# Optimization experiments

Measured on AMD Instinct MI355X. Metric: run time of the kernel, lower is better.

Reference implementation:

```python
import jax, jax.numpy as jnp
import numpy as np

K = 3  # kernel_size


def conv2d_same(x, w, b):
    # x: NHWC, w: HWIO
    y = jax.lax.conv_general_dilated(
        x, w, window_strides=(1, 1), padding='SAME',
        dimension_numbers=('NHWC', 'HWIO', 'NHWC'))
    return y + b


def setup_inputs() -> dict:
    key = jax.random.key(0)
    k0, k1, k2 = jax.random.split(key, 3)
    B, H, Wd, C, F = 8, 128, 128, 64, 128
    x = jax.random.normal(k0, (B, H, Wd, C), jnp.float32)
    # offset conv: small random weights (zeros in original init -> degenerate),
    # scaled down so offsets stay in a realistic few-pixel range
    W_off = jax.random.normal(k1, (K, K, C, 2 * K * K), jnp.float32) * 0.01
    b_off = jnp.zeros((2 * K * K,), jnp.float32)
    fan_in = K * K * K * K * C
    W = jax.random.normal(k2, (K, K, K * K * C, F), jnp.float32) / np.float32(np.sqrt(fan_in))
    b = jnp.zeros((F,), jnp.float32)
    return {"x": x, "W_off": W_off, "b_off": b_off, "W": W, "b": b}


def reference(x, W_off, b_off, W, b):
    B, H, Wd, C = x.shape
    KK = K * K
    # predicted per-pixel, per-tap (dx, dy) offsets
    offsets = conv2d_same(x, W_off, b_off).reshape(B, H, Wd, KK, 2)

    # base pixel grid, stacked as (x, y) like the original
    gy, gx = jnp.meshgrid(jnp.arange(H, dtype=jnp.float32),
                          jnp.arange(Wd, dtype=jnp.float32), indexing='ij')
    grid = jnp.stack([gx, gy], axis=-1)[None, :, :, None, :]  # (1,H,W,1,2)

    # kernel tap grid, 'xy' meshgrid like tf.meshgrid default
    off = (K - 1) / 2.0
    lin = jnp.linspace(-off, off, K).astype(jnp.float32)
    kx, ky = jnp.meshgrid(lin, lin)
    kgrid = jnp.stack([kx, ky], axis=-1).reshape(1, 1, 1, KK, 2)

    loc = grid + kgrid + offsets  # (B,H,W,KK,2)
    lx = jnp.clip(loc[..., 0], 0.0, Wd - 1.0)
    ly = jnp.clip(loc[..., 1], 0.0, H - 1.0)

    x0 = jnp.clip(jnp.floor(lx), 0.0, Wd - 1.0)
    x1 = jnp.clip(jnp.floor(lx) + 1.0, 0.0, Wd - 1.0)
    y0 = jnp.clip(jnp.floor(ly), 0.0, H - 1.0)
    y1 = jnp.clip(jnp.floor(ly) + 1.0, 0.0, H - 1.0)

    # weights computed from the CLIPPED corner coords, as in the original
    wa = (x1 - lx) * (y1 - ly)
    wb = (x1 - lx) * (ly - y0)
    wc = (lx - x0) * (y1 - ly)
    wd = (lx - x0) * (ly - y0)

    x0i, x1i = x0.astype(jnp.int32), x1.astype(jnp.int32)
    y0i, y1i = y0.astype(jnp.int32), y1.astype(jnp.int32)

    xf = x.reshape(B, H * Wd, C)

    def gather(yi, xi):
        idx = (yi * Wd + xi).reshape(B, -1)           # (B, H*W*KK)
        g = jax.vmap(lambda f, i: f[i])(xf, idx)      # (B, P, C)
        return g.reshape(B, H, Wd, KK, C)

    Ia = gather(y0i, x0i)
    Ib = gather(y1i, x0i)
    Ic = gather(y0i, x1i)
    Id = gather(y1i, x1i)

    sampled = (wa[..., None] * Ia + wb[..., None] * Ib
               + wc[..., None] * Ic + wd[..., None] * Id)
    sampled = sampled.reshape(B, H, Wd, KK * C)
    return conv2d_same(sampled, W, b)
```

## Files before the change

### kernel.cpp

```cpp
#include <hip/hip_runtime.h>
#include <hip/hip_bf16.h>

#define B_   8
#define H_   128
#define W_   128
#define C_   64
#define F_   128
#define KDIM 5184
#define BHW_ 131072

#define TH   8
#define TW   16
#define HY   10
#define HX   18
#define NPX  180

#define STILE 0
#define BTILE 11520
#define PARMW 36096
#define PARMO 37536
#define LDSSZ 38976

typedef __bf16 bf16x8 __attribute__((ext_vector_type(8)));
typedef float  f32x4  __attribute__((ext_vector_type(4)));

__device__ __forceinline__ unsigned short f2bf(float f) {
  unsigned int u = __float_as_uint(f);
  unsigned int r = (u + 0x7fffu + ((u >> 16) & 1u)) >> 16;
  return (unsigned short)r;
}

__global__ __launch_bounds__(256) void woff_prep_kernel(
    const float* __restrict__ Woff, unsigned short* __restrict__ WbHi,
    unsigned short* __restrict__ WbLo) {
  int u = blockIdx.x * 256 + threadIdx.x;
  if (u >= 18432) return;
  int j  = u & 7;
  int kq = (u >> 3) & 3;
  int n  = (u >> 5) & 15;
  int nt = (u >> 9) & 1;
  int tc = u >> 10;
  int tap = tc >> 1, kch = tc & 1;
  int o = nt * 16 + n;
  int c = kch * 32 + kq * 8 + j;
  float val = 0.f;
  if (o < 18) val = Woff[(tap * 64 + c) * 18 + o];
  unsigned short h = f2bf(val);
  float hf = __uint_as_float((unsigned)h << 16);
  WbHi[u] = h;
  WbLo[u] = f2bf(val - hf);
}

__global__ __launch_bounds__(256, 3) void offs_mfma_kernel(
    const float* __restrict__ x, const unsigned short* __restrict__ WbHi,
    const unsigned short* __restrict__ WbLo, const float* __restrict__ boff,
    float* __restrict__ offsP) {
  __shared__ __align__(16) short lds[26112];
  const int tid = threadIdx.x, lane = tid & 63, w = tid >> 6;
  const int bid = blockIdx.x;
  const int b  = bid >> 7;
  const int t  = bid & 127;
  const int r4 = t >> 2, cq = t & 3;
  const int gy0 = r4 * 4, gx0 = cq * 32;
  const float* xb = x + (size_t)b * (H_ * W_ * C_);

#pragma unroll
  for (int it = 0; it < 7; ++it) {
    int u = it * 256 + tid;
    if (u < 1632) {
      int p = u >> 3, j = u & 7;
      int rowi = p / 34, coli = p - rowi * 34;
      int gy = gy0 - 1 + rowi, gx = gx0 - 1 + coli;
      union { unsigned short s[8]; uint4 v; } hi, lo;
      if ((unsigned)gy < (unsigned)H_ && (unsigned)gx < (unsigned)W_) {
        const float* src = xb + (((gy << 7) + gx) << 6) + j * 8;
        float4 v0 = ((const float4*)src)[0], v1 = ((const float4*)src)[1];
        float f[8] = {v0.x, v0.y, v0.z, v0.w, v1.x, v1.y, v1.z, v1.w};
#pragma unroll
        for (int e = 0; e < 8; ++e) {
          unsigned short h16 = f2bf(f[e]);
          hi.s[e] = h16;
          lo.s[e] = f2bf(f[e] - __uint_as_float((unsigned)h16 << 16));
        }
      } else {
        hi.v = make_uint4(0, 0, 0, 0);
        lo.v = hi.v;
      }
      int a = p * 64 + ((j ^ (coli & 7)) * 8);
      *(uint4*)&lds[a] = hi.v;
      *(uint4*)&lds[13056 + a] = lo.v;
    }
  }
  __syncthreads();

  const int l15 = lane & 15, kq = lane >> 4;
  const int bbase = (l15 * 4 + kq) * 8;
  f32x4 acc[2][2] = {};

#pragma unroll
  for (int ky = 0; ky < 3; ++ky) {
#pragma unroll
    for (int kx = 0; kx < 3; ++kx) {
      const int tap = ky * 3 + kx;
#pragma unroll
      for (int kch = 0; kch < 2; ++kch) {
        const int tc = tap * 2 + kch;
        bf16x8 bh0 = *(const bf16x8*)&WbHi[tc * 1024 + bbase];
        bf16x8 bh1 = *(const bf16x8*)&WbHi[tc * 1024 + 512 + bbase];
        bf16x8 bl0 = *(const bf16x8*)&WbLo[tc * 1024 + bbase];
        bf16x8 bl1 = *(const bf16x8*)&WbLo[tc * 1024 + 512 + bbase];
#pragma unroll
        for (int mt = 0; mt < 2; ++mt) {
          int coli = mt * 16 + l15 + kx;
          int px = (w + ky) * 34 + coli;
          int a = px * 64 + (((kch * 4 + kq) ^ (coli & 7)) * 8);
          bf16x8 ah = *(const bf16x8*)&lds[a];
          bf16x8 al = *(const bf16x8*)&lds[13056 + a];
          acc[mt][0] = __builtin_amdgcn_mfma_f32_16x16x32_bf16(ah, bh0, acc[mt][0], 0, 0, 0);
          acc[mt][0] = __builtin_amdgcn_mfma_f32_16x16x32_bf16(al, bh0, acc[mt][0], 0, 0, 0);
          acc[mt][0] = __builtin_amdgcn_mfma_f32_16x16x32_bf16(ah, bl0, acc[mt][0], 0, 0, 0);
          acc[mt][1] = __builtin_amdgcn_mfma_f32_16x16x32_bf16(ah, bh1, acc[mt][1], 0, 0, 0);
          acc[mt][1] = __builtin_amdgcn_mfma_f32_16x16x32_bf16(al, bh1, acc[mt][1], 0, 0, 0);
          acc[mt][1] = __builtin_amdgcn_mfma_f32_16x16x32_bf16(ah, bl1, acc[mt][1], 0, 0, 0);
        }
      }
    }
  }

  __syncthreads();
  float* accbuf = (float*)lds;
  float bv0 = boff[l15];
  float bv1 = boff[min(16 + l15, 17)];
#pragma unroll
  for (int mt = 0; mt < 2; ++mt)
#pragma unroll
    for (int r = 0; r < 4; ++r) {
      int px = mt * 16 + kq * 4 + r;
      accbuf[(w * 32 + px) * 19 + l15] = acc[mt][0][r] + bv0;
      if (l15 < 2)
        accbuf[(w * 32 + px) * 19 + 16 + l15] = acc[mt][1][r] + bv1;
    }
  __syncthreads();
  const int lane32 = tid & 31, tpi = tid >> 5;
#pragma unroll
  for (int v = 0; v < 9; ++v) {
    int u = v * 8 + tpi;
    int o = u >> 2, w2 = u & 3;
    float val = accbuf[(w2 * 32 + lane32) * 19 + o];
    offsP[(size_t)o * BHW_ + (size_t)b * 16384 + (gy0 + w2) * 128 + gx0 + lane32] = val;
  }
}

__global__ __launch_bounds__(256) void wt_prep_kernel(
    const float* __restrict__ Wf, unsigned short* __restrict__ Wt) {
  __shared__ float Wl[64][65];
  const int tid = threadIdx.x;
  const int kk0 = (blockIdx.x % 81) * 64;
  const int f0  = (blockIdx.x / 81) * 64;
  for (int i = tid; i < 4096; i += 256) {
    int kk = i >> 6, f = i & 63;
    Wl[kk][f] = Wf[(size_t)(kk0 + kk) * F_ + f0 + f];
  }
  __syncthreads();
  for (int i = tid; i < 4096; i += 256) {
    int f = i >> 6, kk = i & 63;
    Wt[(size_t)(f0 + f) * KDIM + kk0 + kk] = f2bf(Wl[kk][f]);
  }
}

__global__ __launch_bounds__(256, 2) void fused_kernel(
    const float* __restrict__ x, const float* __restrict__ offsP,
    const unsigned short* __restrict__ Wt, const float* __restrict__ bias,
    float* __restrict__ out) {
  __shared__ __align__(16) short lds[LDSSZ];
  const int tid  = threadIdx.x;
  const int lane = tid & 63;
  const int wv   = tid >> 6;
  const int gr   = (blockIdx.x & 7) * 128 + (blockIdx.x >> 3);
  const int b    = gr >> 7;
  const int tile = gr & 127;
  const int ty   = tile >> 3, tx = tile & 7;
  const int gy0  = ty * TH, gx0 = tx * TW;
  const float* xb = x + (size_t)b * (H_ * W_ * C_);

  const int l15  = lane & 15, quad = lane >> 4;
  const int sub  = lane & 7,  rig  = lane >> 3;
  const int wm   = (wv >> 1) * 64, wn = (wv & 1) * 64;

  f32x4 acc[4][4] = {};

  int p0[4];
#pragma unroll
  for (int i = 0; i < 4; ++i) p0[i] = ((wv >> 1) * 4 + i) * HX + l15;
  int bo[2][4];
#pragma unroll
  for (int ks = 0; ks < 2; ++ks)
#pragma unroll
    for (int j = 0; j < 4; ++j)
      bo[ks][j] = BTILE + (wn + 16 * j + l15) * 64 + (((ks * 4 + quad) ^ (l15 & 7)) * 8);

  const int s_py = tid / HX, s_px = tid - s_py * HX;

  for (int t = 0; t < 9; ++t) {
    __syncthreads();
    if (tid < NPX) {
      int gy = gy0 + s_py - 1, gx = gx0 + s_px - 1;
      float wa = 0.f, wb = 0.f, wc = 0.f, wd = 0.f;
      int oA = 0, oB = 0, oC = 0, oD = 0;
      if ((unsigned)gy < (unsigned)H_ && (unsigned)gx < (unsigned)W_) {
        int pix = (b * H_ + gy) * W_ + gx;
        float offx = offsP[(size_t)(2 * t) * BHW_ + pix];
        float offy = offsP[(size_t)(2 * t + 1) * BHW_ + pix];
        float lx = (float)gx + (float)(t % 3 - 1) + offx;
        float ly = (float)gy + (float)(t / 3 - 1) + offy;
        lx = fminf(fmaxf(lx, 0.f), 127.f);
        ly = fminf(fmaxf(ly, 0.f), 127.f);
        float fx = floorf(lx), fy = floorf(ly);
        float x0c = fminf(fmaxf(fx, 0.f), 127.f);
        float x1c = fminf(fmaxf(fx + 1.f, 0.f), 127.f);
        float y0c = fminf(fmaxf(fy, 0.f), 127.f);
        float y1c = fminf(fmaxf(fy + 1.f, 0.f), 127.f);
        wa = (x1c - lx) * (y1c - ly);
        wb = (x1c - lx) * (ly - y0c);
        wc = (lx - x0c) * (y1c - ly);
        wd = (lx - x0c) * (ly - y0c);
        int ix0 = (int)x0c, ix1 = (int)x1c, iy0 = (int)y0c, iy1 = (int)y1c;
        oA = (iy0 * W_ + ix0) * C_;
        oB = (iy1 * W_ + ix0) * C_;
        oC = (iy0 * W_ + ix1) * C_;
        oD = (iy1 * W_ + ix1) * C_;
      }
      ((float4*)&lds[PARMW])[tid] = make_float4(wa, wb, wc, wd);
      ((int4*)&lds[PARMO])[tid]  = make_int4(oA | (s_px << 20), oB, oC, oD);
    }
    __syncthreads();
#pragma unroll
    for (int it = 0; it < 6; ++it) {
      int u = it * 256 + tid;
      if (u < NPX * 8) {
        int p = u >> 3, j = u & 7;
        float4 wv4 = ((const float4*)&lds[PARMW])[p];
        int4   ov4 = ((const int4*)&lds[PARMO])[p];
        int pxl = ov4.x >> 20;
        const float* pa = xb + (ov4.x & 0xFFFFF) + j * 8;
        const float* pb = xb + ov4.y + j * 8;
        const float* pc = xb + ov4.z + j * 8;
        const float* pd = xb + ov4.w + j * 8;
        float4 A0 = ((const float4*)pa)[0], A1 = ((const float4*)pa)[1];
        float4 B0 = ((const float4*)pb)[0], B1 = ((const float4*)pb)[1];
        float4 C0 = ((const float4*)pc)[0], C1 = ((const float4*)pc)[1];
        float4 D0 = ((const float4*)pd)[0], D1 = ((const float4*)pd)[1];
        union { unsigned short s[8]; uint4 v; } uu;
        uu.s[0] = f2bf(wv4.x * A0.x + wv4.y * B0.x + wv4.z * C0.x + wv4.w * D0.x);
        uu.s[1] = f2bf(wv4.x * A0.y + wv4.y * B0.y + wv4.z * C0.y + wv4.w * D0.y);
        uu.s[2] = f2bf(wv4.x * A0.z + wv4.y * B0.z + wv4.z * C0.z + wv4.w * D0.z);
        uu.s[3] = f2bf(wv4.x * A0.w + wv4.y * B0.w + wv4.z * C0.w + wv4.w * D0.w);
        uu.s[4] = f2bf(wv4.x * A1.x + wv4.y * B1.x + wv4.z * C1.x + wv4.w * D1.x);
        uu.s[5] = f2bf(wv4.x * A1.y + wv4.y * B1.y + wv4.z * C1.y + wv4.w * D1.y);
        uu.s[6] = f2bf(wv4.x * A1.z + wv4.y * B1.z + wv4.z * C1.z + wv4.w * D1.z);
        uu.s[7] = f2bf(wv4.x * A1.w + wv4.y * B1.w + wv4.z * C1.w + wv4.w * D1.w);
        *(uint4*)&lds[STILE + p * 64 + ((j ^ (pxl & 7)) * 8)] = uu.v;
      }
    }
    for (int g = 0; g < 3; ++g) {
      __syncthreads();
#pragma unroll
      for (int i = 0; i < 12; ++i) {
        int slot = wv * 12 + i;
        int chunk = slot >> 4;
        int f = ((slot & 15) * 8) + rig;
        int tap2 = g * 3 + chunk;
        const short* src = (const short*)Wt + (size_t)f * KDIM +
                           tap2 * 576 + t * 64 + ((sub ^ rig) * 8);
        __builtin_amdgcn_global_load_lds(
            (const __attribute__((address_space(1))) void*)src,
            (__attribute__((address_space(3))) void*)&lds[BTILE + slot * 512],
            16, 0, 0);
      }
      __syncthreads();
      const int off2 = g * HX;
#pragma unroll
      for (int c3 = 0; c3 < 3; ++c3) {
        int t1 = (l15 + c3) & 7;
        int xr0 = ((quad ^ t1) * 8);
        int xr1 = (((4 + quad) ^ t1) * 8);
#pragma unroll
        for (int ks = 0; ks < 2; ++ks) {
          int xr = ks ? xr1 : xr0;
          bf16x8 af[4], bfr[4];
#pragma unroll
          for (int i = 0; i < 4; ++i)
            af[i] = *(const bf16x8*)&lds[(p0[i] + off2 + c3) * 64 + xr];
#pragma unroll
          for (int j = 0; j < 4; ++j)
            bfr[j] = *(const bf16x8*)&lds[bo[ks][j] + c3 * 8192];
#pragma unroll
          for (int i = 0; i < 4; ++i)
#pragma unroll
            for (int j = 0; j < 4; ++j)
              acc[i][j] = __builtin_amdgcn_mfma_f32_16x16x32_bf16(
                  af[i], bfr[j], acc[i][j], 0, 0, 0);
        }
      }
    }
  }

  float bj[4];
#pragma unroll
  for (int j = 0; j < 4; ++j) bj[j] = bias[wn + 16 * j + l15];
#pragma unroll
  for (int i = 0; i < 4; ++i) {
    int gy = gy0 + (wv >> 1) * 4 + i;
#pragma unroll
    for (int r = 0; r < 4; ++r) {
      int gx = gx0 + quad * 4 + r;
      float* rp = out + ((size_t)((b * H_ + gy) * W_ + gx)) * F_;
#pragma unroll
      for (int j = 0; j < 4; ++j)
        rp[wn + 16 * j + l15] = acc[i][j][r] + bj[j];
    }
  }
}

extern "C" void kernel_launch(void* const* d_in, const int* in_sizes, int n_in,
                              void* d_out, int out_size, void* d_ws, size_t ws_size,
                              hipStream_t stream) {
  (void)in_sizes; (void)n_in; (void)out_size; (void)ws_size;
  const float* x    = (const float*)d_in[0];
  const float* Woff = (const float*)d_in[1];
  const float* boff = (const float*)d_in[2];
  const float* Wf   = (const float*)d_in[3];
  const float* bias = (const float*)d_in[4];
  float* out = (float*)d_out;

  char* ws = (char*)d_ws;
  size_t off_bytes = (size_t)18 * BHW_ * 4;
  size_t p1 = (off_bytes + 255) & ~(size_t)255;
  size_t wt_bytes = (size_t)F_ * KDIM * 2;
  float*          offsP = (float*)ws;
  unsigned short* Wt    = (unsigned short*)(ws + p1);
  unsigned short* WbHi  = (unsigned short*)(ws + p1 + wt_bytes);
  unsigned short* WbLo  = WbHi + 18432;

  woff_prep_kernel<<<72, 256, 0, stream>>>(Woff, WbHi, WbLo);
  offs_mfma_kernel<<<1024, 256, 0, stream>>>(x, WbHi, WbLo, boff, offsP);
  wt_prep_kernel<<<162, 256, 0, stream>>>(Wf, Wt);
  fused_kernel<<<1024, 256, 0, stream>>>(x, offsP, Wt, bias, out);
}
```

Before: 306.5 us.

## Double tile height to 16 rows and double-buffer weight tiles in LDS

Each block of the fused kernel now covers a 16x16 output tile with 512 threads (8 waves) instead of 8x16 with 256. Each weight slice loaded into LDS is therefore reused across twice as many output pixels, and the halo overhead of the sampled input tile shrinks. Weight tiles are double-buffered: the next tap group is prefetched with global_load_lds while MFMAs run on the current one, which also removes a barrier per group. The cost is about 150KB of LDS per block, so only one block fits per CU, and the grid drops to 512 blocks.

```diff
diff --git a/kernel.cpp b/kernel.cpp
--- a/kernel.cpp
+++ b/kernel.cpp
@@ -9,17 +9,18 @@
 #define KDIM 5184
 #define BHW_ 131072
 
-#define TH   8
+#define TH   16
 #define TW   16
-#define HY   10
+#define HY   18
 #define HX   18
-#define NPX  180
+#define NPX  324
 
 #define STILE 0
-#define BTILE 11520
-#define PARMW 36096
-#define PARMO 37536
-#define LDSSZ 38976
+#define BT0   20736
+#define BT1   45312
+#define PARMW 69888
+#define PARMO 72480
+#define LDSSZ 75072
 
 typedef __bf16 bf16x8 __attribute__((ext_vector_type(8)));
 typedef float  f32x4  __attribute__((ext_vector_type(4)));
@@ -168,7 +169,7 @@
   }
 }
 
-__global__ __launch_bounds__(256, 2) void fused_kernel(
+__global__ __launch_bounds__(512, 1) void fused_kernel(
     const float* __restrict__ x, const float* __restrict__ offsP,
     const unsigned short* __restrict__ Wt, const float* __restrict__ bias,
     float* __restrict__ out) {
@@ -176,28 +177,29 @@
   const int tid  = threadIdx.x;
   const int lane = tid & 63;
   const int wv   = tid >> 6;
-  const int gr   = (blockIdx.x & 7) * 128 + (blockIdx.x >> 3);
-  const int b    = gr >> 7;
-  const int tile = gr & 127;
+  const int gr   = (blockIdx.x & 7) * 64 + (blockIdx.x >> 3);
+  const int b    = gr >> 6;
+  const int tile = gr & 63;
   const int ty   = tile >> 3, tx = tile & 7;
   const int gy0  = ty * TH, gx0 = tx * TW;
   const float* xb = x + (size_t)b * (H_ * W_ * C_);
 
   const int l15  = lane & 15, quad = lane >> 4;
   const int sub  = lane & 7,  rig  = lane >> 3;
-  const int wm   = (wv >> 1) * 64, wn = (wv & 1) * 64;
+  const int wn   = (wv & 1) * 64;
+  const int wmr  = (wv >> 1) * 4;
 
   f32x4 acc[4][4] = {};
 
   int p0[4];
 #pragma unroll
-  for (int i = 0; i < 4; ++i) p0[i] = ((wv >> 1) * 4 + i) * HX + l15;
+  for (int i = 0; i < 4; ++i) p0[i] = (wmr + i) * HX + l15;
   int bo[2][4];
 #pragma unroll
   for (int ks = 0; ks < 2; ++ks)
 #pragma unroll
     for (int j = 0; j < 4; ++j)
-      bo[ks][j] = BTILE + (wn + 16 * j + l15) * 64 + (((ks * 4 + quad) ^ (l15 & 7)) * 8);
+      bo[ks][j] = (wn + 16 * j + l15) * 64 + (((ks * 4 + quad) ^ (l15 & 7)) * 8);
 
   const int s_py = tid / HX, s_px = tid - s_py * HX;
 
@@ -233,10 +235,26 @@
       ((float4*)&lds[PARMW])[tid] = make_float4(wa, wb, wc, wd);
       ((int4*)&lds[PARMO])[tid]  = make_int4(oA | (s_px << 20), oB, oC, oD);
     }
+    {
+      const int bt = ((t * 3) & 1) ? BT1 : BT0;
+#pragma unroll
+      for (int i = 0; i < 6; ++i) {
+        int slot = wv * 6 + i;
+        int chunk = slot >> 4;
+        int f = ((slot & 15) * 8) + rig;
+        int tap2 = 0 * 3 + chunk;
+        const short* src = (const short*)Wt + (size_t)f * KDIM +
+                           tap2 * 576 + t * 64 + ((sub ^ rig) * 8);
+        __builtin_amdgcn_global_load_lds(
+            (const __attribute__((address_space(1))) void*)src,
+            (__attribute__((address_space(3))) void*)&lds[bt + slot * 512],
+            16, 0, 0);
+      }
+    }
     __syncthreads();
 #pragma unroll
     for (int it = 0; it < 6; ++it) {
-      int u = it * 256 + tid;
+      int u = it * 512 + tid;
       if (u < NPX * 8) {
         int p = u >> 3, j = u & 7;
         float4 wv4 = ((const float4*)&lds[PARMW])[p];
@@ -262,22 +280,27 @@
         *(uint4*)&lds[STILE + p * 64 + ((j ^ (pxl & 7)) * 8)] = uu.v;
       }
     }
+    __syncthreads();
+
     for (int g = 0; g < 3; ++g) {
-      __syncthreads();
-#pragma unroll
-      for (int i = 0; i < 12; ++i) {
-        int slot = wv * 12 + i;
-        int chunk = slot >> 4;
-        int f = ((slot & 15) * 8) + rig;
-        int tap2 = g * 3 + chunk;
-        const short* src = (const short*)Wt + (size_t)f * KDIM +
-                           tap2 * 576 + t * 64 + ((sub ^ rig) * 8);
-        __builtin_amdgcn_global_load_lds(
-            (const __attribute__((address_space(1))) void*)src,
-            (__attribute__((address_space(3))) void*)&lds[BTILE + slot * 512],
-            16, 0, 0);
-      }
-      __syncthreads();
+      const int s = t * 3 + g;
+      const int bt_cur = (s & 1) ? BT1 : BT0;
+      if (g < 2) {
+        const int bt_nxt = (s & 1) ? BT0 : BT1;
+#pragma unroll
+        for (int i = 0; i < 6; ++i) {
+          int slot = wv * 6 + i;
+          int chunk = slot >> 4;
+          int f = ((slot & 15) * 8) + rig;
+          int tap2 = (g + 1) * 3 + chunk;
+          const short* src = (const short*)Wt + (size_t)f * KDIM +
+                             tap2 * 576 + t * 64 + ((sub ^ rig) * 8);
+          __builtin_amdgcn_global_load_lds(
+              (const __attribute__((address_space(1))) void*)src,
+              (__attribute__((address_space(3))) void*)&lds[bt_nxt + slot * 512],
+              16, 0, 0);
+        }
+      }
       const int off2 = g * HX;
 #pragma unroll
       for (int c3 = 0; c3 < 3; ++c3) {
@@ -293,7 +316,7 @@
             af[i] = *(const bf16x8*)&lds[(p0[i] + off2 + c3) * 64 + xr];
 #pragma unroll
           for (int j = 0; j < 4; ++j)
-            bfr[j] = *(const bf16x8*)&lds[bo[ks][j] + c3 * 8192];
+            bfr[j] = *(const bf16x8*)&lds[bt_cur + bo[ks][j] + c3 * 8192];
 #pragma unroll
           for (int i = 0; i < 4; ++i)
 #pragma unroll
@@ -302,6 +325,7 @@
                   af[i], bfr[j], acc[i][j], 0, 0, 0);
         }
       }
+      if (g < 2) __syncthreads();
     }
   }
 
@@ -310,7 +334,7 @@
   for (int j = 0; j < 4; ++j) bj[j] = bias[wn + 16 * j + l15];
 #pragma unroll
   for (int i = 0; i < 4; ++i) {
-    int gy = gy0 + (wv >> 1) * 4 + i;
+    int gy = gy0 + wmr + i;
 #pragma unroll
     for (int r = 0; r < 4; ++r) {
       int gx = gx0 + quad * 4 + r;
@@ -345,5 +369,5 @@
   woff_prep_kernel<<<72, 256, 0, stream>>>(Woff, WbHi, WbLo);
   offs_mfma_kernel<<<1024, 256, 0, stream>>>(x, WbHi, WbLo, boff, offsP);
   wt_prep_kernel<<<162, 256, 0, stream>>>(Wf, Wt);
-  fused_kernel<<<1024, 256, 0, stream>>>(x, offsP, Wt, bias, out);
-}
+  fused_kernel<<<512, 512, 0, stream>>>(x, offsP, Wt, bias, out);
+}
```

After: 303.1 us. Within noise of the previous version (-1.1%).

## Pre-pack weights into MFMA fragment layout and load B directly from global

Applied to the files above, without the earlier changes.

The weight-prep kernel now writes the main conv weights in a packed per-(tap, tap2) slab layout that matches the MFMA B-fragment ordering. The fused kernel then reads B fragments straight from global/L2 instead of staging them through LDS with global_load_lds and two barriers per group. This shrinks LDS use from about 78KB to about 29KB per block, and launch bounds are raised to allow 4 blocks per CU. The trade-off is that B fragment loads now have global-memory latency inside the MFMA loop, and each wave reads weights redundantly without LDS sharing.

```diff
diff --git a/kernel.cpp b/kernel.cpp
--- a/kernel.cpp
+++ b/kernel.cpp
@@ -16,10 +16,9 @@
 #define NPX  180
 
 #define STILE 0
-#define BTILE 11520
-#define PARMW 36096
-#define PARMO 37536
-#define LDSSZ 38976
+#define PARMW 11520
+#define PARMO 12960
+#define LDSSZ 14400
 
 typedef __bf16 bf16x8 __attribute__((ext_vector_type(8)));
 typedef float  f32x4  __attribute__((ext_vector_type(4)));
@@ -152,25 +151,34 @@
 }
 
 __global__ __launch_bounds__(256) void wt_prep_kernel(
-    const float* __restrict__ Wf, unsigned short* __restrict__ Wt) {
-  __shared__ float Wl[64][65];
-  const int tid = threadIdx.x;
-  const int kk0 = (blockIdx.x % 81) * 64;
-  const int f0  = (blockIdx.x / 81) * 64;
-  for (int i = tid; i < 4096; i += 256) {
-    int kk = i >> 6, f = i & 63;
-    Wl[kk][f] = Wf[(size_t)(kk0 + kk) * F_ + f0 + f];
+    const float* __restrict__ Wf, unsigned short* __restrict__ Wp) {
+  __shared__ __align__(16) unsigned short lt[128][64];
+  const int tid  = threadIdx.x;
+  const int slab = blockIdx.x;
+  const int t = slab / 9, tap2 = slab % 9;
+  const size_t kkb = (size_t)tap2 * 576 + t * 64;
+  {
+    const int kl = tid >> 2, f0 = (tid & 3) * 32;
+    const float* src = Wf + (kkb + kl) * 128 + f0;
+#pragma unroll
+    for (int u = 0; u < 32; ++u)
+      lt[f0 + u][kl] = f2bf(src[u]);
   }
   __syncthreads();
-  for (int i = tid; i < 4096; i += 256) {
-    int f = i >> 6, kk = i & 63;
-    Wt[(size_t)(f0 + f) * KDIM + kk0 + kk] = f2bf(Wl[kk][f]);
-  }
-}
-
-__global__ __launch_bounds__(256, 2) void fused_kernel(
+#pragma unroll
+  for (int k = 0; k < 4; ++k) {
+    int idx = k * 256 + tid;
+    int rec = idx >> 6, rem = idx & 63;
+    int q = rem >> 4, l = rem & 15;
+    int nblk = rec & 7, ks = rec >> 3;
+    uint4 v = *(const uint4*)&lt[nblk * 16 + l][(ks * 4 + q) * 8];
+    *(uint4*)&Wp[(size_t)slab * 8192 + idx * 8] = v;
+  }
+}
+
+__global__ __launch_bounds__(256, 4) void fused_kernel(
     const float* __restrict__ x, const float* __restrict__ offsP,
-    const unsigned short* __restrict__ Wt, const float* __restrict__ bias,
+    const unsigned short* __restrict__ Wp, const float* __restrict__ bias,
     float* __restrict__ out) {
   __shared__ __align__(16) short lds[LDSSZ];
   const int tid  = threadIdx.x;
@@ -184,20 +192,13 @@
   const float* xb = x + (size_t)b * (H_ * W_ * C_);
 
   const int l15  = lane & 15, quad = lane >> 4;
-  const int sub  = lane & 7,  rig  = lane >> 3;
-  const int wm   = (wv >> 1) * 64, wn = (wv & 1) * 64;
+  const int nh   = wv & 1, wn = nh * 64;
 
   f32x4 acc[4][4] = {};
 
   int p0[4];
 #pragma unroll
   for (int i = 0; i < 4; ++i) p0[i] = ((wv >> 1) * 4 + i) * HX + l15;
-  int bo[2][4];
-#pragma unroll
-  for (int ks = 0; ks < 2; ++ks)
-#pragma unroll
-    for (int j = 0; j < 4; ++j)
-      bo[ks][j] = BTILE + (wn + 16 * j + l15) * 64 + (((ks * 4 + quad) ^ (l15 & 7)) * 8);
 
   const int s_py = tid / HX, s_px = tid - s_py * HX;
 
@@ -262,38 +263,26 @@
         *(uint4*)&lds[STILE + p * 64 + ((j ^ (pxl & 7)) * 8)] = uu.v;
       }
     }
+    __syncthreads();
+
+    const unsigned short* wpt = Wp + (size_t)t * (9 * 8192) + (size_t)lane * 8;
+#pragma unroll
     for (int g = 0; g < 3; ++g) {
-      __syncthreads();
-#pragma unroll
-      for (int i = 0; i < 12; ++i) {
-        int slot = wv * 12 + i;
-        int chunk = slot >> 4;
-        int f = ((slot & 15) * 8) + rig;
-        int tap2 = g * 3 + chunk;
-        const short* src = (const short*)Wt + (size_t)f * KDIM +
-                           tap2 * 576 + t * 64 + ((sub ^ rig) * 8);
-        __builtin_amdgcn_global_load_lds(
-            (const __attribute__((address_space(1))) void*)src,
-            (__attribute__((address_space(3))) void*)&lds[BTILE + slot * 512],
-            16, 0, 0);
-      }
-      __syncthreads();
       const int off2 = g * HX;
 #pragma unroll
       for (int c3 = 0; c3 < 3; ++c3) {
+        const unsigned short* wpg = wpt + (g * 3 + c3) * 8192;
         int t1 = (l15 + c3) & 7;
-        int xr0 = ((quad ^ t1) * 8);
-        int xr1 = (((4 + quad) ^ t1) * 8);
 #pragma unroll
         for (int ks = 0; ks < 2; ++ks) {
-          int xr = ks ? xr1 : xr0;
+          int xr = ((ks * 4 + quad) ^ t1) * 8;
           bf16x8 af[4], bfr[4];
+#pragma unroll
+          for (int j = 0; j < 4; ++j)
+            bfr[j] = *(const bf16x8*)&wpg[(ks * 8 + nh * 4 + j) * 512];
 #pragma unroll
           for (int i = 0; i < 4; ++i)
             af[i] = *(const bf16x8*)&lds[(p0[i] + off2 + c3) * 64 + xr];
-#pragma unroll
-          for (int j = 0; j < 4; ++j)
-            bfr[j] = *(const bf16x8*)&lds[bo[ks][j] + c3 * 8192];
 #pragma unroll
           for (int i = 0; i < 4; ++i)
 #pragma unroll
@@ -336,14 +325,14 @@
   char* ws = (char*)d_ws;
   size_t off_bytes = (size_t)18 * BHW_ * 4;
   size_t p1 = (off_bytes + 255) & ~(size_t)255;
-  size_t wt_bytes = (size_t)F_ * KDIM * 2;
+  size_t wp_bytes = (size_t)81 * 8192 * 2;
   float*          offsP = (float*)ws;
-  unsigned short* Wt    = (unsigned short*)(ws + p1);
-  unsigned short* WbHi  = (unsigned short*)(ws + p1 + wt_bytes);
+  unsigned short* Wp    = (unsigned short*)(ws + p1);
+  unsigned short* WbHi  = (unsigned short*)(ws + p1 + wp_bytes);
   unsigned short* WbLo  = WbHi + 18432;
 
   woff_prep_kernel<<<72, 256, 0, stream>>>(Woff, WbHi, WbLo);
   offs_mfma_kernel<<<1024, 256, 0, stream>>>(x, WbHi, WbLo, boff, offsP);
-  wt_prep_kernel<<<162, 256, 0, stream>>>(Wf, Wt);
-  fused_kernel<<<1024, 256, 0, stream>>>(x, offsP, Wt, bias, out);
-}
+  wt_prep_kernel<<<81, 256, 0, stream>>>(Wf, Wp);
+  fused_kernel<<<1024, 256, 0, stream>>>(x, offsP, Wp, bias, out);
+}
```

Measured after the change: 391.3 us. 1.28x slower.

## Precompute quantized bilinear sampling params in offset kernel and overlap weight loads

Applied to the files above, without the earlier changes.

The offset-conv kernel now computes the bilinear corner index and the four interpolation weights itself, packing them into a 16-byte record per pixel and tap (weights quantized to 16-bit fixed point). The fused kernel drops the per-tap parameter stage and its LDS staging plus one barrier, and reads the packed record directly in the gather loop. Weight-tile loads for the first group are issued before the gather, and later groups load after compute, which cuts barriers. The trade-offs are a larger workspace write and read (16 B versus 8 B per pixel-tap), 16-bit weight quantization error, and redundant parameter decoding by the 8 threads that share a pixel.

```diff
diff --git a/kernel.cpp b/kernel.cpp
--- a/kernel.cpp
+++ b/kernel.cpp
@@ -17,9 +17,7 @@
 
 #define STILE 0
 #define BTILE 11520
-#define PARMW 36096
-#define PARMO 37536
-#define LDSSZ 38976
+#define LDSSZ 36096
 
 typedef __bf16 bf16x8 __attribute__((ext_vector_type(8)));
 typedef float  f32x4  __attribute__((ext_vector_type(4)));
@@ -54,7 +52,7 @@
 __global__ __launch_bounds__(256, 3) void offs_mfma_kernel(
     const float* __restrict__ x, const unsigned short* __restrict__ WbHi,
     const unsigned short* __restrict__ WbLo, const float* __restrict__ boff,
-    float* __restrict__ offsP) {
+    uint4* __restrict__ paramsQ) {
   __shared__ __align__(16) short lds[26112];
   const int tid = threadIdx.x, lane = tid & 63, w = tid >> 6;
   const int bid = blockIdx.x;
@@ -141,13 +139,39 @@
         accbuf[(w * 32 + px) * 19 + 16 + l15] = acc[mt][1][r] + bv1;
     }
   __syncthreads();
-  const int lane32 = tid & 31, tpi = tid >> 5;
-#pragma unroll
-  for (int v = 0; v < 9; ++v) {
-    int u = v * 8 + tpi;
-    int o = u >> 2, w2 = u & 3;
-    float val = accbuf[(w2 * 32 + lane32) * 19 + o];
-    offsP[(size_t)o * BHW_ + (size_t)b * 16384 + (gy0 + w2) * 128 + gx0 + lane32] = val;
+#pragma unroll
+  for (int k = 0; k < 5; ++k) {
+    int u = k * 256 + tid;
+    if (u < 1152) {
+      int tt  = u >> 7;
+      int w2  = (u >> 5) & 3, l32 = u & 31;
+      int pxl = w2 * 32 + l32;
+      float offx = accbuf[pxl * 19 + 2 * tt];
+      float offy = accbuf[pxl * 19 + 2 * tt + 1];
+      int gy = gy0 + w2, gx = gx0 + l32;
+      int kxo = tt - (tt / 3) * 3 - 1;
+      int kyo = tt / 3 - 1;
+      float lx = fminf(fmaxf((float)(gx + kxo) + offx, 0.f), 127.f);
+      float ly = fminf(fmaxf((float)(gy + kyo) + offy, 0.f), 127.f);
+      float fx = floorf(lx), fy = floorf(ly);
+      float x1c = fminf(fx + 1.f, 127.f);
+      float y1c = fminf(fy + 1.f, 127.f);
+      float wa = (x1c - lx) * (y1c - ly);
+      float wb = (x1c - lx) * (ly - fy);
+      float wc = (lx - fx) * (y1c - ly);
+      float wd = (lx - fx) * (ly - fy);
+      int ix0 = (int)fx, iy0 = (int)fy;
+      unsigned dx = (x1c > fx) ? 1u : 0u;
+      unsigned dy = (y1c > fy) ? 1u : 0u;
+      uint4 enc;
+      enc.x = (unsigned)((iy0 * 128 + ix0) * 64) | (dx << 20) | (dy << 21);
+      enc.y = (unsigned)(wa * 65535.f + 0.5f) |
+              ((unsigned)(wb * 65535.f + 0.5f) << 16);
+      enc.z = (unsigned)(wc * 65535.f + 0.5f) |
+              ((unsigned)(wd * 65535.f + 0.5f) << 16);
+      enc.w = 0;
+      paramsQ[(size_t)tt * BHW_ + b * 16384 + gy * 128 + gx] = enc;
+    }
   }
 }
 
@@ -169,7 +193,7 @@
 }
 
 __global__ __launch_bounds__(256, 2) void fused_kernel(
-    const float* __restrict__ x, const float* __restrict__ offsP,
+    const float* __restrict__ x, const uint4* __restrict__ paramsQ,
     const unsigned short* __restrict__ Wt, const float* __restrict__ bias,
     float* __restrict__ out) {
   __shared__ __align__(16) short lds[LDSSZ];
@@ -185,7 +209,7 @@
 
   const int l15  = lane & 15, quad = lane >> 4;
   const int sub  = lane & 7,  rig  = lane >> 3;
-  const int wm   = (wv >> 1) * 64, wn = (wv & 1) * 64;
+  const int wn   = (wv & 1) * 64;
 
   f32x4 acc[4][4] = {};
 
@@ -199,85 +223,65 @@
     for (int j = 0; j < 4; ++j)
       bo[ks][j] = BTILE + (wn + 16 * j + l15) * 64 + (((ks * 4 + quad) ^ (l15 & 7)) * 8);
 
-  const int s_py = tid / HX, s_px = tid - s_py * HX;
-
   for (int t = 0; t < 9; ++t) {
     __syncthreads();
-    if (tid < NPX) {
-      int gy = gy0 + s_py - 1, gx = gx0 + s_px - 1;
-      float wa = 0.f, wb = 0.f, wc = 0.f, wd = 0.f;
-      int oA = 0, oB = 0, oC = 0, oD = 0;
-      if ((unsigned)gy < (unsigned)H_ && (unsigned)gx < (unsigned)W_) {
-        int pix = (b * H_ + gy) * W_ + gx;
-        float offx = offsP[(size_t)(2 * t) * BHW_ + pix];
-        float offy = offsP[(size_t)(2 * t + 1) * BHW_ + pix];
-        float lx = (float)gx + (float)(t % 3 - 1) + offx;
-        float ly = (float)gy + (float)(t / 3 - 1) + offy;
-        lx = fminf(fmaxf(lx, 0.f), 127.f);
-        ly = fminf(fmaxf(ly, 0.f), 127.f);
-        float fx = floorf(lx), fy = floorf(ly);
-        float x0c = fminf(fmaxf(fx, 0.f), 127.f);
-        float x1c = fminf(fmaxf(fx + 1.f, 0.f), 127.f);
-        float y0c = fminf(fmaxf(fy, 0.f), 127.f);
-        float y1c = fminf(fmaxf(fy + 1.f, 0.f), 127.f);
-        wa = (x1c - lx) * (y1c - ly);
-        wb = (x1c - lx) * (ly - y0c);
-        wc = (lx - x0c) * (y1c - ly);
-        wd = (lx - x0c) * (ly - y0c);
-        int ix0 = (int)x0c, ix1 = (int)x1c, iy0 = (int)y0c, iy1 = (int)y1c;
-        oA = (iy0 * W_ + ix0) * C_;
-        oB = (iy1 * W_ + ix0) * C_;
-        oC = (iy0 * W_ + ix1) * C_;
-        oD = (iy1 * W_ + ix1) * C_;
-      }
-      ((float4*)&lds[PARMW])[tid] = make_float4(wa, wb, wc, wd);
-      ((int4*)&lds[PARMO])[tid]  = make_int4(oA | (s_px << 20), oB, oC, oD);
-    }
-    __syncthreads();
+#pragma unroll
+    for (int i = 0; i < 12; ++i) {
+      int slot = wv * 12 + i;
+      int chunk = slot >> 4;
+      int f = ((slot & 15) * 8) + rig;
+      const short* src = (const short*)Wt + (size_t)f * KDIM +
+                         chunk * 576 + t * 64 + ((sub ^ rig) * 8);
+      __builtin_amdgcn_global_load_lds(
+          (const __attribute__((address_space(1))) void*)src,
+          (__attribute__((address_space(3))) void*)&lds[BTILE + slot * 512],
+          16, 0, 0);
+    }
 #pragma unroll
     for (int it = 0; it < 6; ++it) {
       int u = it * 256 + tid;
       if (u < NPX * 8) {
         int p = u >> 3, j = u & 7;
-        float4 wv4 = ((const float4*)&lds[PARMW])[p];
-        int4   ov4 = ((const int4*)&lds[PARMO])[p];
-        int pxl = ov4.x >> 20;
-        const float* pa = xb + (ov4.x & 0xFFFFF) + j * 8;
-        const float* pb = xb + ov4.y + j * 8;
-        const float* pc = xb + ov4.z + j * 8;
-        const float* pd = xb + ov4.w + j * 8;
-        float4 A0 = ((const float4*)pa)[0], A1 = ((const float4*)pa)[1];
-        float4 B0 = ((const float4*)pb)[0], B1 = ((const float4*)pb)[1];
-        float4 C0 = ((const float4*)pc)[0], C1 = ((const float4*)pc)[1];
-        float4 D0 = ((const float4*)pd)[0], D1 = ((const float4*)pd)[1];
-        union { unsigned short s[8]; uint4 v; } uu;
-        uu.s[0] = f2bf(wv4.x * A0.x + wv4.y * B0.x + wv4.z * C0.x + wv4.w * D0.x);
-        uu.s[1] = f2bf(wv4.x * A0.y + wv4.y * B0.y + wv4.z * C0.y + wv4.w * D0.y);
-        uu.s[2] = f2bf(wv4.x * A0.z + wv4.y * B0.z + wv4.z * C0.z + wv4.w * D0.z);
-        uu.s[3] = f2bf(wv4.x * A0.w + wv4.y * B0.w + wv4.z * C0.w + wv4.w * D0.w);
-        uu.s[4] = f2bf(wv4.x * A1.x + wv4.y * B1.x + wv4.z * C1.x + wv4.w * D1.x);
-        uu.s[5] = f2bf(wv4.x * A1.y + wv4.y * B1.y + wv4.z * C1.y + wv4.w * D1.y);
-        uu.s[6] = f2bf(wv4.x * A1.z + wv4.y * B1.z + wv4.z * C1.z + wv4.w * D1.z);
-        uu.s[7] = f2bf(wv4.x * A1.w + wv4.y * B1.w + wv4.z * C1.w + wv4.w * D1.w);
-        *(uint4*)&lds[STILE + p * 64 + ((j ^ (pxl & 7)) * 8)] = uu.v;
-      }
-    }
+        int rowi = (p * 456) >> 13;
+        int coli = p - rowi * 18;
+        int gy = gy0 + rowi - 1, gx = gx0 + coli - 1;
+        uint4 sv = make_uint4(0, 0, 0, 0);
+        if ((unsigned)gy < (unsigned)H_ && (unsigned)gx < (unsigned)W_) {
+          int pix = (b * H_ + gy) * W_ + gx;
+          uint4 pr = paramsQ[(size_t)t * BHW_ + pix];
+          int oA  = pr.x & 0xFFFFF;
+          int dxo = ((pr.x >> 20) & 1) << 6;
+          int dyo = ((pr.x >> 21) & 1) << 13;
+          const float s = 1.f / 65535.f;
+          float wa = (float)(pr.y & 0xFFFF) * s;
+          float wb = (float)(pr.y >> 16) * s;
+          float wc = (float)(pr.z & 0xFFFF) * s;
+          float wd = (float)(pr.z >> 16) * s;
+          const float* pa = xb + oA + j * 8;
+          const float* pb = pa + dyo;
+          const float* pc = pa + dxo;
+          const float* pd = pc + dyo;
+          float4 A0 = ((const float4*)pa)[0], A1 = ((const float4*)pa)[1];
+          float4 B0 = ((const float4*)pb)[0], B1 = ((const float4*)pb)[1];
+          float4 C0 = ((const float4*)pc)[0], C1 = ((const float4*)pc)[1];
+          float4 D0 = ((const float4*)pd)[0], D1 = ((const float4*)pd)[1];
+          union { __bf16 h[8]; uint4 v; } uu;
+          uu.h[0] = (__bf16)(wa * A0.x + wb * B0.x + wc * C0.x + wd * D0.x);
+          uu.h[1] = (__bf16)(wa * A0.y + wb * B0.y + wc * C0.y + wd * D0.y);
+          uu.h[2] = (__bf16)(wa * A0.z + wb * B0.z + wc * C0.z + wd * D0.z);
+          uu.h[3] = (__bf16)(wa * A0.w + wb * B0.w + wc * C0.w + wd * D0.w);
+          uu.h[4] = (__bf16)(wa * A1.x + wb * B1.x + wc * C1.x + wd * D1.x);
+          uu.h[5] = (__bf16)(wa * A1.y + wb * B1.y + wc * C1.y + wd * D1.y);
+          uu.h[6] = (__bf16)(wa * A1.z + wb * B1.z + wc * C1.z + wd * D1.z);
+          uu.h[7] = (__bf16)(wa * A1.w + wb * B1.w + wc * C1.w + wd * D1.w);
+          sv = uu.v;
+        }
+        *(uint4*)&lds[STILE + p * 64 + ((j ^ (coli & 7)) * 8)] = sv;
+      }
+    }
+    __syncthreads();
+
     for (int g = 0; g < 3; ++g) {
-      __syncthreads();
-#pragma unroll
-      for (int i = 0; i < 12; ++i) {
-        int slot = wv * 12 + i;
-        int chunk = slot >> 4;
-        int f = ((slot & 15) * 8) + rig;
-        int tap2 = g * 3 + chunk;
-        const short* src = (const short*)Wt + (size_t)f * KDIM +
-                           tap2 * 576 + t * 64 + ((sub ^ rig) * 8);
-        __builtin_amdgcn_global_load_lds(
-            (const __attribute__((address_space(1))) void*)src,
-            (__attribute__((address_space(3))) void*)&lds[BTILE + slot * 512],
-            16, 0, 0);
-      }
-      __syncthreads();
       const int off2 = g * HX;
 #pragma unroll
       for (int c3 = 0; c3 < 3; ++c3) {
@@ -301,6 +305,23 @@
               acc[i][j] = __builtin_amdgcn_mfma_f32_16x16x32_bf16(
                   af[i], bfr[j], acc[i][j], 0, 0, 0);
         }
+      }
+      if (g < 2) {
+        __syncthreads();
+#pragma unroll
+        for (int i = 0; i < 12; ++i) {
+          int slot = wv * 12 + i;
+          int chunk = slot >> 4;
+          int f = ((slot & 15) * 8) + rig;
+          int tap2 = (g + 1) * 3 + chunk;
+          const short* src = (const short*)Wt + (size_t)f * KDIM +
+                             tap2 * 576 + t * 64 + ((sub ^ rig) * 8);
+          __builtin_amdgcn_global_load_lds(
+              (const __attribute__((address_space(1))) void*)src,
+              (__attribute__((address_space(3))) void*)&lds[BTILE + slot * 512],
+              16, 0, 0);
+        }
+        __syncthreads();
       }
     }
   }
@@ -334,16 +355,15 @@
   float* out = (float*)d_out;
 
   char* ws = (char*)d_ws;
-  size_t off_bytes = (size_t)18 * BHW_ * 4;
-  size_t p1 = (off_bytes + 255) & ~(size_t)255;
+  size_t pq_bytes = (size_t)9 * BHW_ * 16;
   size_t wt_bytes = (size_t)F_ * KDIM * 2;
-  float*          offsP = (float*)ws;
-  unsigned short* Wt    = (unsigned short*)(ws + p1);
-  unsigned short* WbHi  = (unsigned short*)(ws + p1 + wt_bytes);
-  unsigned short* WbLo  = WbHi + 18432;
+  uint4*          paramsQ = (uint4*)ws;
+  unsigned short* Wt      = (unsigned short*)(ws + pq_bytes);
+  unsigned short* WbHi    = (unsigned short*)(ws + pq_bytes + wt_bytes);
+  unsigned short* WbLo    = WbHi + 18432;
 
   woff_prep_kernel<<<72, 256, 0, stream>>>(Woff, WbHi, WbLo);
-  offs_mfma_kernel<<<1024, 256, 0, stream>>>(x, WbHi, WbLo, boff, offsP);
+  offs_mfma_kernel<<<1024, 256, 0, stream>>>(x, WbHi, WbLo, boff, paramsQ);
   wt_prep_kernel<<<162, 256, 0, stream>>>(Wf, Wt);
-  fused_kernel<<<1024, 256, 0, stream>>>(x, offsP, Wt, bias, out);
-}
+  fused_kernel<<<1024, 256, 0, stream>>>(x, paramsQ, Wt, bias, out);
+}
```

Result: slower. 314.7 us (+2.6%).
